# Kernel tuning notes

Hardware: AMD Instinct MI355X
Metric: run time of the kernel (lower is better)

## Reference

```python
import jax, jax.numpy as jnp
import numpy as np

N_NODES = 100000


def setup_inputs() -> dict:
    key = jax.random.key(0)
    k1, k2, k3 = jax.random.split(key, 3)
    emb = jax.random.normal(k1, (N_NODES, 64), dtype=jnp.float32)
    src = jax.random.randint(k2, (1250000,), 0, N_NODES, dtype=jnp.int64)
    dst = jax.random.randint(k3, (1250000,), 0, N_NODES, dtype=jnp.int64)
    return {"emb": emb, "src": src, "dst": dst}


def reference(emb, src, dst):
    # DGL GraphConv(norm='both', weight=False, bias=False):
    #   out = D_in^{-1/2} * A * (D_out^{-1/2} * emb), degrees clamped to >= 1.
    n = emb.shape[0]
    e = src.shape[0]
    ones = jnp.ones((e,), dtype=emb.dtype)
    out_deg = jax.ops.segment_sum(ones, src, num_segments=n)  # out-degree of src nodes
    in_deg = jax.ops.segment_sum(ones, dst, num_segments=n)   # in-degree of dst nodes
    src_norm = jnp.clip(out_deg, 1.0, None) ** -0.5           # [N]
    dst_norm = jnp.clip(in_deg, 1.0, None) ** -0.5            # [N]
    h = emb * src_norm[:, None]                               # [N, D] pre-normalize
    msg = h[src]                                              # [E, D] gather
    agg = jax.ops.segment_sum(msg, dst, num_segments=n)       # [N, D] scatter-add
    return agg * dst_norm[:, None]
```

## Files before the change

kernel.cpp:

```cpp
#include <hip/hip_runtime.h>
#include <hip/hip_fp16.h>

#define NNODES 100000
#define DIM 64
#define TILE 256
#define NTILES ((NNODES + TILE - 1) / TILE)
#define NTPAD 392
#define CAP 4608
#define EPT 16
#define BIN_THREADS 512
#define BIN_CHUNK (BIN_THREADS * EPT)

__global__ void convert_kernel(const float* __restrict__ emb, const float* __restrict__ src_norm,
                               __half* __restrict__ embh, int total8) {
    int i = blockIdx.x * blockDim.x + threadIdx.x;
    if (i < total8) {
        int base = i * 8;
        float w = src_norm[base >> 6];
        float4 a = *(const float4*)(emb + base);
        float4 b = *(const float4*)(emb + base + 4);
        __half2* o = (__half2*)(embh + base);
        o[0] = __floats2half2_rn(a.x * w, a.y * w);
        o[1] = __floats2half2_rn(a.z * w, a.w * w);
        o[2] = __floats2half2_rn(b.x * w, b.y * w);
        o[3] = __floats2half2_rn(b.z * w, b.w * w);
    } else if (i - total8 < 8) {
        int k = i - total8;
        __half2* o = (__half2*)(embh + (size_t)NNODES * DIM + k * 8);
        __half2 z = __floats2half2_rn(0.0f, 0.0f);
        o[0] = z; o[1] = z; o[2] = z; o[3] = z;
    }
}

__global__ __launch_bounds__(BIN_THREADS) void bin_kernel(
        const int* __restrict__ src, const int* __restrict__ dst,
        int* __restrict__ gcurD, int* __restrict__ gcurS,
        unsigned int* __restrict__ binnedD, int* __restrict__ binnedS, int E) {
    __shared__ int histD[NTPAD], histS[NTPAD], baseD[NTPAD], baseS[NTPAD];
    __shared__ unsigned short rankD[BIN_CHUNK], rankS[BIN_CHUNK];
    int tid = threadIdx.x;
    for (int t = tid; t < NTPAD; t += BIN_THREADS) { histD[t] = 0; histS[t] = 0; }
    __syncthreads();
    int base = blockIdx.x * BIN_CHUNK;
    #pragma unroll
    for (int i = 0; i < EPT; i++) {
        int idx = base + i * BIN_THREADS + tid;
        if (idx < E) {
            int d = dst[idx];
            int s = src[idx];
            rankD[i * BIN_THREADS + tid] = (unsigned short)atomicAdd(&histD[d >> 8], 1);
            rankS[i * BIN_THREADS + tid] = (unsigned short)atomicAdd(&histS[s >> 8], 1);
        }
    }
    __syncthreads();
    for (int t = tid; t < NTPAD; t += BIN_THREADS) {
        int h = histD[t];
        baseD[t] = h ? atomicAdd(&gcurD[t], h) : 0;
        h = histS[t];
        baseS[t] = h ? atomicAdd(&gcurS[t], h) : 0;
    }
    __syncthreads();
    #pragma unroll
    for (int i = 0; i < EPT; i++) {
        int idx = base + i * BIN_THREADS + tid;
        if (idx < E) {
            int d = dst[idx];
            int s = src[idx];
            int tD = d >> 8, tS = s >> 8;
            int pD = baseD[tD] + (int)rankD[i * BIN_THREADS + tid];
            int pS = baseS[tS] + (int)rankS[i * BIN_THREADS + tid];
            if (pD < CAP) binnedD[(size_t)tD * CAP + pD] = ((unsigned)(d & 255) << 17) | (unsigned)s;
            if (pS < CAP) binnedS[(size_t)tS * CAP + pS] = s;
        }
    }
}

__global__ __launch_bounds__(256) void sortnorm_kernel(
        const int* __restrict__ gcurS, const int* __restrict__ binnedS,
        const int* __restrict__ gcurD, const unsigned int* __restrict__ binnedD,
        float* __restrict__ src_norm, int* __restrict__ sortedD,
        int* __restrict__ offs, int* __restrict__ deg) {
    __shared__ int cnt[TILE];
    __shared__ int cur[TILE];
    __shared__ int wsum[4];
    __shared__ int tot_s;
    int t = blockIdx.x, tid = threadIdx.x;
    int node = t * TILE + tid;
    cnt[tid] = 0;
    __syncthreads();
    {
        int lenS = min(gcurS[t], CAP);
        const int* segS = binnedS + (size_t)t * CAP;
        for (int j = tid; j < lenS; j += 256)
            atomicAdd(&cnt[segS[j] & 255], 1);
    }
    __syncthreads();
    if (node < NNODES)
        src_norm[node] = rsqrtf(fmaxf((float)cnt[tid], 1.0f));
    __syncthreads();
    cnt[tid] = 0;
    __syncthreads();
    int len = min(gcurD[t], CAP);
    const unsigned int* seg = binnedD + (size_t)t * CAP;
    for (int j = tid; j < len; j += 256)
        atomicAdd(&cnt[seg[j] >> 17], 1);
    __syncthreads();
    int v = cnt[tid];
    int vpad = (v + 7) & ~7;
    int lane = tid & 63, w = tid >> 6;
    int x = vpad;
    #pragma unroll
    for (int off = 1; off < 64; off <<= 1) {
        int y = __shfl_up(x, off, 64);
        if (lane >= off) x += y;
    }
    if (lane == 63) wsum[w] = x;
    __syncthreads();
    int add = 0;
    #pragma unroll
    for (int k = 0; k < 4; k++) add += (k < w) ? wsum[k] : 0;
    int ex = x - vpad + add;
    cur[tid] = ex;
    if (tid == 255) tot_s = ex + vpad;
    __syncthreads();
    for (int j = tid; j < len; j += 256) {
        unsigned int p = seg[j];
        int dl = p >> 17;
        int pos = atomicAdd(&cur[dl], 1);
        if (pos < CAP) sortedD[(size_t)t * CAP + pos] = (int)(p & 0x1FFFF);
    }
    __syncthreads();
    int pe = ex + vpad;
    for (int p = cur[tid]; p < pe && p < CAP; p++) sortedD[(size_t)t * CAP + p] = NNODES;
    for (int k = tot_s + tid; k < CAP; k += 256) sortedD[(size_t)t * CAP + k] = NNODES;
    if (node < NNODES) {
        offs[node] = t * CAP + ex;
        deg[node] = v;
    }
}

__global__ __launch_bounds__(256) void agg4_kernel(
        const __half* __restrict__ embh, const int* __restrict__ offs,
        const int* __restrict__ deg, const int* __restrict__ sortedD,
        float* __restrict__ out, int n) {
    int wid = threadIdx.x >> 6;
    int lane = threadIdx.x & 63;
    int node = blockIdx.x * 4 + wid;
    if (node >= n) return;
    int m = deg[node];
    const int* run = sortedD + offs[node];
    int slot = lane >> 3;
    int oct = lane & 7;
    float a0 = 0.f, a1 = 0.f, a2 = 0.f, a3 = 0.f, a4 = 0.f, a5 = 0.f, a6 = 0.f, a7 = 0.f;
    for (int j = 0; j < m; j += 8) {
        int idx = run[j + slot];
        float4 hv = *(const float4*)(embh + ((size_t)idx << 6) + (oct << 3));
        const __half2* hp = (const __half2*)&hv;
        float2 f0 = __half22float2(hp[0]);
        float2 f1 = __half22float2(hp[1]);
        float2 f2 = __half22float2(hp[2]);
        float2 f3 = __half22float2(hp[3]);
        a0 += f0.x; a1 += f0.y;
        a2 += f1.x; a3 += f1.y;
        a4 += f2.x; a5 += f2.y;
        a6 += f3.x; a7 += f3.y;
    }
    #pragma unroll
    for (int off = 8; off < 64; off <<= 1) {
        a0 += __shfl_xor(a0, off);
        a1 += __shfl_xor(a1, off);
        a2 += __shfl_xor(a2, off);
        a3 += __shfl_xor(a3, off);
        a4 += __shfl_xor(a4, off);
        a5 += __shfl_xor(a5, off);
        a6 += __shfl_xor(a6, off);
        a7 += __shfl_xor(a7, off);
    }
    float dn = rsqrtf(fmaxf((float)m, 1.0f));
    if (lane < 16) {
        int half = lane >> 3;
        float4 o = half ? make_float4(a4 * dn, a5 * dn, a6 * dn, a7 * dn)
                        : make_float4(a0 * dn, a1 * dn, a2 * dn, a3 * dn);
        *(float4*)(out + ((size_t)node << 6) + (oct << 3) + (half << 2)) = o;
    }
}

extern "C" void kernel_launch(void* const* d_in, const int* in_sizes, int n_in,
                              void* d_out, int out_size, void* d_ws, size_t ws_size,
                              hipStream_t stream) {
    const float* emb = (const float*)d_in[0];
    const int* src = (const int*)d_in[1];
    const int* dst = (const int*)d_in[2];
    int E = in_sizes[1];
    float* out = (float*)d_out;

    int* gcurD = (int*)d_ws;
    int* gcurS = gcurD + NTPAD;
    unsigned int* binnedD = (unsigned int*)(gcurS + NTPAD);
    int* binnedS = (int*)(binnedD + (size_t)NTILES * CAP);
    int* sortedD = binnedS;
    int* offs = binnedS + (size_t)NTILES * CAP;
    int* deg = offs + NNODES;
    float* src_norm = (float*)(deg + NNODES);
    __half* embh = (__half*)(src_norm + NNODES);

    hipMemsetAsync(gcurD, 0, 2 * NTPAD * sizeof(int), stream);

    int bin_blocks = (E + BIN_CHUNK - 1) / BIN_CHUNK;
    bin_kernel<<<bin_blocks, BIN_THREADS, 0, stream>>>(src, dst, gcurD, gcurS, binnedD, binnedS, E);

    sortnorm_kernel<<<NTILES, 256, 0, stream>>>(gcurS, binnedS, gcurD, binnedD,
                                                src_norm, sortedD, offs, deg);

    int total8 = NNODES * DIM / 8;
    convert_kernel<<<(total8 + 8 + 255) / 256, 256, 0, stream>>>(emb, src_norm, embh, total8);

    agg4_kernel<<<(NNODES + 3) / 4, 256, 0, stream>>>(embh, offs, deg, sortedD, out, NNODES);
}
```

Measured before the change: 105.4 us.

## Fuse fp16 conversion into sortnorm kernel and unroll gather loop by two

```diff
diff --git a/kernel.cpp b/kernel.cpp
--- a/kernel.cpp
+++ b/kernel.cpp
@@ -10,27 +10,6 @@
 #define EPT 16
 #define BIN_THREADS 512
 #define BIN_CHUNK (BIN_THREADS * EPT)
-
-__global__ void convert_kernel(const float* __restrict__ emb, const float* __restrict__ src_norm,
-                               __half* __restrict__ embh, int total8) {
-    int i = blockIdx.x * blockDim.x + threadIdx.x;
-    if (i < total8) {
-        int base = i * 8;
-        float w = src_norm[base >> 6];
-        float4 a = *(const float4*)(emb + base);
-        float4 b = *(const float4*)(emb + base + 4);
-        __half2* o = (__half2*)(embh + base);
-        o[0] = __floats2half2_rn(a.x * w, a.y * w);
-        o[1] = __floats2half2_rn(a.z * w, a.w * w);
-        o[2] = __floats2half2_rn(b.x * w, b.y * w);
-        o[3] = __floats2half2_rn(b.z * w, b.w * w);
-    } else if (i - total8 < 8) {
-        int k = i - total8;
-        __half2* o = (__half2*)(embh + (size_t)NNODES * DIM + k * 8);
-        __half2 z = __floats2half2_rn(0.0f, 0.0f);
-        o[0] = z; o[1] = z; o[2] = z; o[3] = z;
-    }
-}
 
 __global__ __launch_bounds__(BIN_THREADS) void bin_kernel(
         const int* __restrict__ src, const int* __restrict__ dst,
@@ -78,10 +57,11 @@
 __global__ __launch_bounds__(256) void sortnorm_kernel(
         const int* __restrict__ gcurS, const int* __restrict__ binnedS,
         const int* __restrict__ gcurD, const unsigned int* __restrict__ binnedD,
-        float* __restrict__ src_norm, int* __restrict__ sortedD,
-        int* __restrict__ offs, int* __restrict__ deg) {
+        const float* __restrict__ emb, __half* __restrict__ embh,
+        int* __restrict__ sortedD, int* __restrict__ offs, int* __restrict__ deg) {
     __shared__ int cnt[TILE];
     __shared__ int cur[TILE];
+    __shared__ float norm_s[TILE];
     __shared__ int wsum[4];
     __shared__ int tot_s;
     int t = blockIdx.x, tid = threadIdx.x;
@@ -95,8 +75,30 @@
             atomicAdd(&cnt[segS[j] & 255], 1);
     }
     __syncthreads();
-    if (node < NNODES)
-        src_norm[node] = rsqrtf(fmaxf((float)cnt[tid], 1.0f));
+    norm_s[tid] = rsqrtf(fmaxf((float)cnt[tid], 1.0f));
+    __syncthreads();
+    {
+        int nrows = min(TILE, NNODES - t * TILE);
+        size_t ebase = (size_t)t * TILE * DIM;
+        int chunks = nrows * (DIM / 8);
+        for (int i = tid; i < chunks; i += 256) {
+            int off8 = i * 8;
+            float w = norm_s[off8 >> 6];
+            float4 a = *(const float4*)(emb + ebase + off8);
+            float4 b = *(const float4*)(emb + ebase + off8 + 4);
+            __half2* o = (__half2*)(embh + ebase + off8);
+            o[0] = __floats2half2_rn(a.x * w, a.y * w);
+            o[1] = __floats2half2_rn(a.z * w, a.w * w);
+            o[2] = __floats2half2_rn(b.x * w, b.y * w);
+            o[3] = __floats2half2_rn(b.z * w, b.w * w);
+        }
+        if (node == NNODES) {
+            __half2 z = __floats2half2_rn(0.0f, 0.0f);
+            __half2* o = (__half2*)(embh + (size_t)NNODES * DIM);
+            #pragma unroll
+            for (int k = 0; k < DIM / 2; k++) o[k] = z;
+        }
+    }
     __syncthreads();
     cnt[tid] = 0;
     __syncthreads();
@@ -148,22 +150,28 @@
     int node = blockIdx.x * 4 + wid;
     if (node >= n) return;
     int m = deg[node];
+    int mp = (m + 7) & ~7;
     const int* run = sortedD + offs[node];
     int slot = lane >> 3;
     int oct = lane & 7;
     float a0 = 0.f, a1 = 0.f, a2 = 0.f, a3 = 0.f, a4 = 0.f, a5 = 0.f, a6 = 0.f, a7 = 0.f;
-    for (int j = 0; j < m; j += 8) {
-        int idx = run[j + slot];
-        float4 hv = *(const float4*)(embh + ((size_t)idx << 6) + (oct << 3));
-        const __half2* hp = (const __half2*)&hv;
-        float2 f0 = __half22float2(hp[0]);
-        float2 f1 = __half22float2(hp[1]);
-        float2 f2 = __half22float2(hp[2]);
-        float2 f3 = __half22float2(hp[3]);
-        a0 += f0.x; a1 += f0.y;
-        a2 += f1.x; a3 += f1.y;
-        a4 += f2.x; a5 += f2.y;
-        a6 += f3.x; a7 += f3.y;
+    for (int j = 0; j < mp; j += 16) {
+        int i0 = run[j + slot];
+        int j2 = j + 8;
+        int i1 = (j2 < mp) ? run[j2 + slot] : NNODES;
+        float4 hv0 = *(const float4*)(embh + ((size_t)i0 << 6) + (oct << 3));
+        float4 hv1 = *(const float4*)(embh + ((size_t)i1 << 6) + (oct << 3));
+        const __half2* h0 = (const __half2*)&hv0;
+        const __half2* h1 = (const __half2*)&hv1;
+        float2 f;
+        f = __half22float2(h0[0]); a0 += f.x; a1 += f.y;
+        f = __half22float2(h0[1]); a2 += f.x; a3 += f.y;
+        f = __half22float2(h0[2]); a4 += f.x; a5 += f.y;
+        f = __half22float2(h0[3]); a6 += f.x; a7 += f.y;
+        f = __half22float2(h1[0]); a0 += f.x; a1 += f.y;
+        f = __half22float2(h1[1]); a2 += f.x; a3 += f.y;
+        f = __half22float2(h1[2]); a4 += f.x; a5 += f.y;
+        f = __half22float2(h1[3]); a6 += f.x; a7 += f.y;
     }
     #pragma unroll
     for (int off = 8; off < 64; off <<= 1) {
@@ -201,8 +209,7 @@
     int* sortedD = binnedS;
     int* offs = binnedS + (size_t)NTILES * CAP;
     int* deg = offs + NNODES;
-    float* src_norm = (float*)(deg + NNODES);
-    __half* embh = (__half*)(src_norm + NNODES);
+    __half* embh = (__half*)(deg + NNODES);
 
     hipMemsetAsync(gcurD, 0, 2 * NTPAD * sizeof(int), stream);
 
@@ -210,10 +217,7 @@
     bin_kernel<<<bin_blocks, BIN_THREADS, 0, stream>>>(src, dst, gcurD, gcurS, binnedD, binnedS, E);
 
     sortnorm_kernel<<<NTILES, 256, 0, stream>>>(gcurS, binnedS, gcurD, binnedD,
-                                                src_norm, sortedD, offs, deg);
-
-    int total8 = NNODES * DIM / 8;
-    convert_kernel<<<(total8 + 8 + 255) / 256, 256, 0, stream>>>(emb, src_norm, embh, total8);
+                                                emb, embh, sortedD, offs, deg);
 
     agg4_kernel<<<(NNODES + 3) / 4, 256, 0, stream>>>(embh, offs, deg, sortedD, out, NNODES);
 }
```

New measurement: 99.97 us. -5.2%, faster.
